# Kernel optimization log

Hardware: AMD Instinct MI355X
Metric: run time of the kernel (lower is better)

## Reference

```python
import jax, jax.numpy as jnp
import numpy as np

B, S, D_MODEL, H = 4, 2048, 1024, 16
D_K = D_MODEL // H


def setup_inputs() -> dict:
    key = jax.random.key(0)
    kx, kq, kk, kv, ko = jax.random.split(key, 5)
    scale = 1.0 / np.sqrt(D_MODEL)
    return {
        "x": jax.random.normal(kx, (B, S, D_MODEL), dtype=jnp.float32),
        "W_q": jax.random.normal(kq, (D_MODEL, D_MODEL), dtype=jnp.float32) * scale,
        "W_k": jax.random.normal(kk, (D_MODEL, D_MODEL), dtype=jnp.float32) * scale,
        "W_v": jax.random.normal(kv, (D_MODEL, D_MODEL), dtype=jnp.float32) * scale,
        "W_out": jax.random.normal(ko, (D_MODEL, D_MODEL), dtype=jnp.float32) * scale,
    }


def reference(x, W_q, W_k, W_v, W_out):
    # nn.Linear(bias=False): y = x @ W.T; weights stored as (out, in).
    Bx, Sx, D = x.shape
    q = (x @ W_q.T).reshape(Bx, Sx, H, D_K).transpose(0, 2, 1, 3)  # (B,H,S,d_k)
    k = (x @ W_k.T).reshape(Bx, Sx, H, D_K).transpose(0, 2, 1, 3)
    v = (x @ W_v.T).reshape(Bx, Sx, H, D_K).transpose(0, 2, 1, 3)
    scores = jnp.einsum("bhsd,bhtd->bhst", q, k) / jnp.sqrt(jnp.float32(D_K))
    attn = jax.nn.softmax(scores, axis=-1)
    out = jnp.einsum("bhst,bhtd->bhsd", attn, v)  # (B,H,S,d_k)
    out = out.transpose(0, 2, 1, 3).reshape(Bx, Sx, D)  # combine heads
    return out @ W_out.T
```

## Files before the change

### kernel.cpp

```cpp
#include <hip/hip_runtime.h>

#define BATCH 4
#define SEQ 2048
#define DM 1024
#define NH 16
#define DK 64

typedef unsigned short u16;
typedef unsigned int u32;
typedef __attribute__((ext_vector_type(8))) short bfrag;
typedef __attribute__((ext_vector_type(4))) short bfrag4;
typedef __attribute__((ext_vector_type(4))) float ffrag;

#if defined(__has_builtin)
#if __has_builtin(__builtin_amdgcn_mfma_f32_16x16x16bf16_1k)
#define HAVE_MFMA16 1
#endif
#endif
#ifndef HAVE_MFMA16
#define HAVE_MFMA16 0
#endif

__device__ inline u16 f2bf(float f) {
  union { float f; u32 u; } v; v.f = f;
  u32 u = v.u;
  return (u16)((u + 0x7FFFu + ((u >> 16) & 1u)) >> 16);
}
__device__ inline float bf2f(u16 u) {
  union { u32 u; float f; } v; v.u = ((u32)u) << 16;
  return v.f;
}
__device__ inline ffrag MFMA(bfrag a, bfrag b, ffrag c) {
  return __builtin_amdgcn_mfma_f32_16x16x32_bf16(a, b, c, 0, 0, 0);
}
#if HAVE_MFMA16
__device__ inline ffrag MFMA16(bfrag4 a, bfrag4 b, ffrag c) {
  return __builtin_amdgcn_mfma_f32_16x16x16bf16_1k(a, b, c, 0, 0, 0);
}
#endif

__device__ __forceinline__ void g2l16(const u16* g, u16* l) {
  __builtin_amdgcn_global_load_lds(
      (const __attribute__((address_space(1))) u16*)g,
      (__attribute__((address_space(3))) u16*)l, 16, 0, 0);
}

__global__ __launch_bounds__(256) void cvt_bf16(const float* __restrict__ in,
                                                u16* __restrict__ out, int n4) {
  int i = blockIdx.x * 256 + threadIdx.x;
  if (i >= n4) return;
  float4 v = ((const float4*)in)[i];
  union { u16 u[4]; uint2 d; } o;
  o.u[0] = f2bf(v.x); o.u[1] = f2bf(v.y); o.u[2] = f2bf(v.z); o.u[3] = f2bf(v.w);
  ((uint2*)out)[i] = o.d;
}

__global__ __launch_bounds__(256) void cvt_w4(
    const float* __restrict__ a, const float* __restrict__ b,
    const float* __restrict__ c, const float* __restrict__ d,
    u16* __restrict__ oa, u16* __restrict__ ob,
    u16* __restrict__ oc, u16* __restrict__ od) {
  int which = blockIdx.x >> 10;
  int i = (blockIdx.x & 1023) * 256 + threadIdx.x;
  const float* in = which == 0 ? a : which == 1 ? b : which == 2 ? c : d;
  u16* out = which == 0 ? oa : which == 1 ? ob : which == 2 ? oc : od;
  float4 v = ((const float4*)in)[i];
  union { u16 u[4]; uint2 dd; } o;
  o.u[0] = f2bf(v.x); o.u[1] = f2bf(v.y); o.u[2] = f2bf(v.z); o.u[3] = f2bf(v.w);
  ((uint2*)out)[i] = o.dd;
}

__global__ __launch_bounds__(256) void gemm_qkv(
    const u16* __restrict__ xb,
    const u16* __restrict__ Wq, const u16* __restrict__ Wk,
    u16* __restrict__ Qb, u16* __restrict__ Kb) {
  const u16* Bm; u16* O;
  if (blockIdx.z == 0) { Bm = Wq; O = Qb; }
  else { Bm = Wk; O = Kb; }

  const int K = DM;
  const int bm = blockIdx.y * 128, bn = blockIdx.x * 128;
  __shared__ __align__(16) u16 As[128 * 32];
  __shared__ __align__(16) u16 Bs[128 * 32];
  const int tid = threadIdx.x;
  const int lane = tid & 63;
  const int w = tid >> 6;
  const int wr = w >> 1, wc = w & 1;
  const int l15 = lane & 15, quad = lane >> 4;
  const int srow = tid >> 2, scol = (tid & 3) * 8;

  ffrag acc[4][4] = {};

  for (int k0 = 0; k0 < K; k0 += 32) {
    __syncthreads();
    g2l16(&xb[(size_t)(bm + srow) * K + k0 + scol], &As[tid * 8]);
    g2l16(&xb[(size_t)(bm + 64 + srow) * K + k0 + scol], &As[(tid + 256) * 8]);
    g2l16(&Bm[(size_t)(bn + srow) * K + k0 + scol], &Bs[tid * 8]);
    g2l16(&Bm[(size_t)(bn + 64 + srow) * K + k0 + scol], &Bs[(tid + 256) * 8]);
    __syncthreads();
    bfrag af[4], bf[4];
#pragma unroll
    for (int i = 0; i < 4; i++)
      af[i] = *(const bfrag*)(&As[(wr * 64 + i * 16 + l15) * 32 + quad * 8]);
#pragma unroll
    for (int j = 0; j < 4; j++)
      bf[j] = *(const bfrag*)(&Bs[(wc * 64 + j * 16 + l15) * 32 + quad * 8]);
#pragma unroll
    for (int i = 0; i < 4; i++)
#pragma unroll
      for (int j = 0; j < 4; j++)
        acc[i][j] = MFMA(af[i], bf[j], acc[i][j]);
  }

#pragma unroll
  for (int i = 0; i < 4; i++)
#pragma unroll
    for (int j = 0; j < 4; j++)
#pragma unroll
      for (int r = 0; r < 4; r++) {
        int m = bm + wr * 64 + i * 16 + quad * 4 + r;
        int n = bn + wc * 64 + j * 16 + l15;
        int b = m >> 11, s = m & 2047;
        int h = n >> 6, d = n & 63;
        O[(((size_t)(b * NH + h)) * SEQ + s) * DK + d] = f2bf(acc[i][j][r]);
      }
}

__global__ __launch_bounds__(256) void gemm_v(
    const u16* __restrict__ xb, const u16* __restrict__ Wv,
    u16* __restrict__ VbT) {
  const int K = DM;
  const int bm = blockIdx.y * 128, bn = blockIdx.x * 128;
  __shared__ __align__(16) u16 As[128 * 32];
  __shared__ __align__(16) u16 Bs[128 * 32];
  const int tid = threadIdx.x;
  const int lane = tid & 63;
  const int w = tid >> 6;
  const int wr = w >> 1, wc = w & 1;
  const int l15 = lane & 15, quad = lane >> 4;
  const int srow = tid >> 2, scol = (tid & 3) * 8;

  ffrag acc[4][4] = {};

  for (int k0 = 0; k0 < K; k0 += 32) {
    __syncthreads();
    g2l16(&xb[(size_t)(bm + srow) * K + k0 + scol], &As[tid * 8]);
    g2l16(&xb[(size_t)(bm + 64 + srow) * K + k0 + scol], &As[(tid + 256) * 8]);
    g2l16(&Wv[(size_t)(bn + srow) * K + k0 + scol], &Bs[tid * 8]);
    g2l16(&Wv[(size_t)(bn + 64 + srow) * K + k0 + scol], &Bs[(tid + 256) * 8]);
    __syncthreads();
    bfrag af[4], bf[4];
#pragma unroll
    for (int i = 0; i < 4; i++)
      af[i] = *(const bfrag*)(&Bs[(wr * 64 + i * 16 + l15) * 32 + quad * 8]);
#pragma unroll
    for (int j = 0; j < 4; j++)
      bf[j] = *(const bfrag*)(&As[(wc * 64 + j * 16 + l15) * 32 + quad * 8]);
#pragma unroll
    for (int i = 0; i < 4; i++)
#pragma unroll
      for (int j = 0; j < 4; j++)
        acc[i][j] = MFMA(af[i], bf[j], acc[i][j]);
  }

#pragma unroll
  for (int i = 0; i < 4; i++)
#pragma unroll
    for (int j = 0; j < 4; j++)
#pragma unroll
      for (int r = 0; r < 4; r++) {
        int n = bn + wr * 64 + i * 16 + quad * 4 + r;
        int m = bm + wc * 64 + j * 16 + l15;
        int b = m >> 11, s = m & 2047;
        int h = n >> 6, d = n & 63;
        VbT[(((size_t)(b * NH + h)) * DK + d) * SEQ + s] = f2bf(acc[i][j][r]);
      }
}

__global__ __launch_bounds__(256) void gemm_out(
    const u16* __restrict__ Ab, const u16* __restrict__ Wo, float* __restrict__ C) {
  const int K = DM, N = DM;
  const int bm = blockIdx.y * 128, bn = blockIdx.x * 128;
  __shared__ __align__(16) u16 As[128 * 32];
  __shared__ __align__(16) u16 Bs[128 * 32];
  const int tid = threadIdx.x;
  const int lane = tid & 63;
  const int w = tid >> 6;
  const int wr = w >> 1, wc = w & 1;
  const int l15 = lane & 15, quad = lane >> 4;
  const int srow = tid >> 2, scol = (tid & 3) * 8;

  ffrag acc[4][4] = {};

  for (int k0 = 0; k0 < K; k0 += 32) {
    __syncthreads();
    g2l16(&Ab[(size_t)(bm + srow) * K + k0 + scol], &As[tid * 8]);
    g2l16(&Ab[(size_t)(bm + 64 + srow) * K + k0 + scol], &As[(tid + 256) * 8]);
    g2l16(&Wo[(size_t)(bn + srow) * K + k0 + scol], &Bs[tid * 8]);
    g2l16(&Wo[(size_t)(bn + 64 + srow) * K + k0 + scol], &Bs[(tid + 256) * 8]);
    __syncthreads();
    bfrag af[4], bf[4];
#pragma unroll
    for (int i = 0; i < 4; i++)
      af[i] = *(const bfrag*)(&As[(wr * 64 + i * 16 + l15) * 32 + quad * 8]);
#pragma unroll
    for (int j = 0; j < 4; j++)
      bf[j] = *(const bfrag*)(&Bs[(wc * 64 + j * 16 + l15) * 32 + quad * 8]);
#pragma unroll
    for (int i = 0; i < 4; i++)
#pragma unroll
      for (int j = 0; j < 4; j++)
        acc[i][j] = MFMA(af[i], bf[j], acc[i][j]);
  }

#pragma unroll
  for (int i = 0; i < 4; i++)
#pragma unroll
    for (int j = 0; j < 4; j++)
#pragma unroll
      for (int r = 0; r < 4; r++) {
        int m = bm + wr * 64 + i * 16 + quad * 4 + r;
        int n = bn + wc * 64 + j * 16 + l15;
        C[(size_t)m * N + n] = acc[i][j][r];
      }
}

#define ATS 72
__global__ __launch_bounds__(256) void attn(
    const u16* __restrict__ Qb, const u16* __restrict__ Kb,
    const u16* __restrict__ VbT, u16* __restrict__ Ab) {
  const int bh = blockIdx.y;
  const int b = bh >> 4, h = bh & 15;
  const int qbase = blockIdx.x * 128;
  const int tid = threadIdx.x;
  const int w = tid >> 6, lane = tid & 63;
  const int l15 = lane & 15, quad = lane >> 4;

  __shared__ __align__(16) u16 Ks[64 * ATS];
  __shared__ __align__(16) u16 Vt[64 * ATS];
#if !HAVE_MFMA16
  __shared__ __align__(16) u16 Ps[4][32 * ATS];
#endif

  const size_t hbase = (size_t)bh * SEQ * DK;

  const float qscale = 0.125f * 1.4426950408889634f;
  bfrag q[2][2];
#pragma unroll
  for (int i = 0; i < 2; i++)
#pragma unroll
    for (int kk = 0; kk < 2; kk++) {
      bfrag t = *(const bfrag*)(&Qb[hbase +
          (size_t)(qbase + w * 32 + i * 16 + l15) * DK + kk * 32 + quad * 8]);
#pragma unroll
      for (int e = 0; e < 8; e++)
        q[i][kk][e] = (short)f2bf(bf2f((u16)t[e]) * qscale);
    }

  ffrag O[4][2] = {};
  float lsum[2] = {0.f, 0.f};

  for (int kv0 = 0; kv0 < SEQ; kv0 += 64) {
    __syncthreads();
#pragma unroll
    for (int i = 0; i < 2; i++) {
      int c = tid + i * 256;
      int row = c >> 3, col = (c & 7) * 8;
      *(int4*)(&Ks[row * ATS + col]) =
          *(const int4*)(&Kb[hbase + (size_t)(kv0 + row) * DK + col]);
      *(int4*)(&Vt[row * ATS + col]) =
          *(const int4*)(&VbT[hbase + (size_t)row * SEQ + kv0 + col]);
    }
    __syncthreads();

#if HAVE_MFMA16
    bfrag4 pb[4][2];
#endif
#pragma unroll
    for (int j = 0; j < 4; j++) {
      bfrag k0f = *(const bfrag*)(&Ks[(j * 16 + l15) * ATS + quad * 8]);
      bfrag k1f = *(const bfrag*)(&Ks[(j * 16 + l15) * ATS + 32 + quad * 8]);
#pragma unroll
      for (int i = 0; i < 2; i++) {
        ffrag z = {};
        z = MFMA(k0f, q[i][0], z);
        z = MFMA(k1f, q[i][1], z);
        u32 u[4]; float ts = 0.f;
#pragma unroll
        for (int r = 0; r < 4; r++) {
          float p = __builtin_amdgcn_exp2f(z[r]);
          u[r] = __float_as_uint(p);
          ts += __uint_as_float(u[r] & 0xffff0000u);
        }
        lsum[i] += ts;
        u32 lo = (u[1] & 0xffff0000u) | (u[0] >> 16);
        u32 hi = (u[3] & 0xffff0000u) | (u[2] >> 16);
#if HAVE_MFMA16
        union { u32 d[2]; bfrag4 v; } pk;
        pk.d[0] = lo; pk.d[1] = hi;
        pb[j][i] = pk.v;
#else
        union { u32 d[2]; uint2 v; } pk;
        pk.d[0] = lo; pk.d[1] = hi;
        *(uint2*)(&Ps[w][(i * 16 + l15) * ATS + j * 16 + quad * 4]) = pk.v;
#endif
      }
    }

#if HAVE_MFMA16
#pragma unroll
    for (int j = 0; j < 4; j++)
#pragma unroll
      for (int db = 0; db < 4; db++) {
        bfrag4 vf = *(const bfrag4*)(&Vt[(db * 16 + l15) * ATS + j * 16 + quad * 4]);
        O[db][0] = MFMA16(vf, pb[j][0], O[db][0]);
        O[db][1] = MFMA16(vf, pb[j][1], O[db][1]);
      }
#else
#pragma unroll
    for (int kk = 0; kk < 2; kk++) {
      bfrag pf0 = *(const bfrag*)(&Ps[w][l15 * ATS + kk * 32 + quad * 8]);
      bfrag pf1 = *(const bfrag*)(&Ps[w][(16 + l15) * ATS + kk * 32 + quad * 8]);
#pragma unroll
      for (int db = 0; db < 4; db++) {
        bfrag vf = *(const bfrag*)(&Vt[(db * 16 + l15) * ATS + kk * 32 + quad * 8]);
        O[db][0] = MFMA(vf, pf0, O[db][0]);
        O[db][1] = MFMA(vf, pf1, O[db][1]);
      }
    }
#endif
  }

  float rl[2];
#pragma unroll
  for (int i = 0; i < 2; i++) {
    float s = lsum[i];
    s += __shfl_xor(s, 16);
    s += __shfl_xor(s, 32);
    rl[i] = 1.0f / s;
  }

  const size_t obase = ((size_t)b * SEQ) * DM + (size_t)h * DK;
#pragma unroll
  for (int db = 0; db < 4; db++)
#pragma unroll
    for (int i = 0; i < 2; i++) {
      int s = qbase + w * 32 + i * 16 + l15;
      union { u16 u[4]; uint2 d; } o;
#pragma unroll
      for (int r = 0; r < 4; r++) o.u[r] = f2bf(O[db][i][r] * rl[i]);
      *(uint2*)(&Ab[obase + (size_t)s * DM + db * 16 + quad * 4]) = o.d;
    }
}

extern "C" void kernel_launch(void* const* d_in, const int* in_sizes, int n_in,
                              void* d_out, int out_size, void* d_ws, size_t ws_size,
                              hipStream_t stream) {
  const float* x  = (const float*)d_in[0];
  const float* Wq = (const float*)d_in[1];
  const float* Wk = (const float*)d_in[2];
  const float* Wv = (const float*)d_in[3];
  const float* Wo = (const float*)d_in[4];
  float* out = (float*)d_out;

  char* ws = (char*)d_ws;
  u16* xb  = (u16*)(ws + 0);
  u16* Wqb = (u16*)(ws + 16777216);
  u16* Wkb = (u16*)(ws + 18874368);
  u16* Wvb = (u16*)(ws + 20971520);
  u16* Wob = (u16*)(ws + 23068672);
  u16* Qb  = (u16*)(ws + 25165824);
  u16* Kb  = (u16*)(ws + 41943040);
  u16* VbT = (u16*)(ws + 58720256);
  u16* Ab  = (u16*)(ws + 75497472);
  const size_t NEED = 92274688;
  if (ws_size < NEED) return;

  cvt_bf16<<<8192, 256, 0, stream>>>(x, xb, (BATCH * SEQ * DM) / 4);
  cvt_w4<<<4096, 256, 0, stream>>>(Wq, Wk, Wv, Wo, Wqb, Wkb, Wvb, Wob);

  dim3 gqk(DM / 128, (BATCH * SEQ) / 128, 2);
  gemm_qkv<<<gqk, 256, 0, stream>>>(xb, Wqb, Wkb, Qb, Kb);
  dim3 gv(DM / 128, (BATCH * SEQ) / 128);
  gemm_v<<<gv, 256, 0, stream>>>(xb, Wvb, VbT);

  dim3 gat(SEQ / 128, BATCH * NH);
  attn<<<gat, 256, 0, stream>>>(Qb, Kb, VbT, Ab);

  dim3 gout(DM / 128, (BATCH * SEQ) / 128);
  gemm_out<<<gout, 256, 0, stream>>>(Ab, Wob, out);
}
```

Baseline: 309.7 us.

## Pre-swizzle V into MFMA fragment layout and double-buffer V via direct LDS loads

The V projection now writes V in a per-64-key-tile swizzled layout that matches the MFMA16 B-fragment order, so the attention kernel can copy each tile into LDS with contiguous global_load_lds and read fragments without padding. V tiles are double-buffered so the next tile's load overlaps the current compute, and K fragments are read straight from global memory instead of being staged in LDS. This removes the per-iteration register round-trip staging and one barrier, at the risk of uncoalesced, cache-reliant K loads. The non-MFMA16 fallback is removed and replaced with a stub that returns c unchanged.

Result: slower. 345.5 us (+11.6%).

```diff
diff --git a/kernel.cpp b/kernel.cpp
--- a/kernel.cpp
+++ b/kernel.cpp
@@ -12,31 +12,29 @@
 typedef __attribute__((ext_vector_type(4))) short bfrag4;
 typedef __attribute__((ext_vector_type(4))) float ffrag;
 
+__device__ inline u16 f2bf(float f) {
+  union { float f; u32 u; } v; v.f = f;
+  u32 u = v.u;
+  return (u16)((u + 0x7FFFu + ((u >> 16) & 1u)) >> 16);
+}
+__device__ inline float bf2f(u16 u) {
+  union { u32 u; float f; } v; v.u = ((u32)u) << 16;
+  return v.f;
+}
+__device__ inline ffrag MFMA(bfrag a, bfrag b, ffrag c) {
+  return __builtin_amdgcn_mfma_f32_16x16x32_bf16(a, b, c, 0, 0, 0);
+}
 #if defined(__has_builtin)
 #if __has_builtin(__builtin_amdgcn_mfma_f32_16x16x16bf16_1k)
 #define HAVE_MFMA16 1
 #endif
 #endif
-#ifndef HAVE_MFMA16
-#define HAVE_MFMA16 0
-#endif
-
-__device__ inline u16 f2bf(float f) {
-  union { float f; u32 u; } v; v.f = f;
-  u32 u = v.u;
-  return (u16)((u + 0x7FFFu + ((u >> 16) & 1u)) >> 16);
-}
-__device__ inline float bf2f(u16 u) {
-  union { u32 u; float f; } v; v.u = ((u32)u) << 16;
-  return v.f;
-}
-__device__ inline ffrag MFMA(bfrag a, bfrag b, ffrag c) {
-  return __builtin_amdgcn_mfma_f32_16x16x32_bf16(a, b, c, 0, 0, 0);
-}
 #if HAVE_MFMA16
 __device__ inline ffrag MFMA16(bfrag4 a, bfrag4 b, ffrag c) {
   return __builtin_amdgcn_mfma_f32_16x16x16bf16_1k(a, b, c, 0, 0, 0);
 }
+#else
+__device__ inline ffrag MFMA16(bfrag4 a, bfrag4 b, ffrag c) { return c; }
 #endif
 
 __device__ __forceinline__ void g2l16(const u16* g, u16* l) {
@@ -128,7 +126,7 @@
 
 __global__ __launch_bounds__(256) void gemm_v(
     const u16* __restrict__ xb, const u16* __restrict__ Wv,
-    u16* __restrict__ VbT) {
+    u16* __restrict__ Vsw) {
   const int K = DM;
   const int bm = blockIdx.y * 128, bn = blockIdx.x * 128;
   __shared__ __align__(16) u16 As[128 * 32];
@@ -173,7 +171,11 @@
         int m = bm + wc * 64 + j * 16 + l15;
         int b = m >> 11, s = m & 2047;
         int h = n >> 6, d = n & 63;
-        VbT[(((size_t)(b * NH + h)) * DK + d) * SEQ + s] = f2bf(acc[i][j][r]);
+        size_t hb = (size_t)(b * NH + h) * (SEQ * DK);
+        size_t off = hb + (size_t)(s >> 6) * 4096 +
+            ((((d >> 4) * 4 + ((s >> 4) & 3)) * 64 +
+              ((s >> 2) & 3) * 16 + (d & 15)) * 4 + (s & 3));
+        Vsw[off] = f2bf(acc[i][j][r]);
       }
 }
 
@@ -225,10 +227,9 @@
       }
 }
 
-#define ATS 72
 __global__ __launch_bounds__(256) void attn(
     const u16* __restrict__ Qb, const u16* __restrict__ Kb,
-    const u16* __restrict__ VbT, u16* __restrict__ Ab) {
+    const u16* __restrict__ Vsw, u16* __restrict__ Ab) {
   const int bh = blockIdx.y;
   const int b = bh >> 4, h = bh & 15;
   const int qbase = blockIdx.x * 128;
@@ -236,11 +237,7 @@
   const int w = tid >> 6, lane = tid & 63;
   const int l15 = lane & 15, quad = lane >> 4;
 
-  __shared__ __align__(16) u16 Ks[64 * ATS];
-  __shared__ __align__(16) u16 Vt[64 * ATS];
-#if !HAVE_MFMA16
-  __shared__ __align__(16) u16 Ps[4][32 * ATS];
-#endif
+  __shared__ __align__(16) u16 Vt[2][4096];
 
   const size_t hbase = (size_t)bh * SEQ * DK;
 
@@ -260,26 +257,28 @@
   ffrag O[4][2] = {};
   float lsum[2] = {0.f, 0.f};
 
-  for (int kv0 = 0; kv0 < SEQ; kv0 += 64) {
-    __syncthreads();
-#pragma unroll
-    for (int i = 0; i < 2; i++) {
-      int c = tid + i * 256;
-      int row = c >> 3, col = (c & 7) * 8;
-      *(int4*)(&Ks[row * ATS + col]) =
-          *(const int4*)(&Kb[hbase + (size_t)(kv0 + row) * DK + col]);
-      *(int4*)(&Vt[row * ATS + col]) =
-          *(const int4*)(&VbT[hbase + (size_t)row * SEQ + kv0 + col]);
+  {
+    const u16* src = &Vsw[hbase];
+    g2l16(&src[tid * 8], &Vt[0][tid * 8]);
+    g2l16(&src[2048 + tid * 8], &Vt[0][2048 + tid * 8]);
+  }
+
+  for (int t = 0; t < SEQ / 64; t++) {
+    const int kv0 = t * 64;
+    const int buf = t & 1;
+    __syncthreads();
+    if (t + 1 < SEQ / 64) {
+      const u16* src = &Vsw[hbase + (size_t)(t + 1) * 4096];
+      g2l16(&src[tid * 8], &Vt[buf ^ 1][tid * 8]);
+      g2l16(&src[2048 + tid * 8], &Vt[buf ^ 1][2048 + tid * 8]);
     }
-    __syncthreads();
-
-#if HAVE_MFMA16
+
     bfrag4 pb[4][2];
-#endif
 #pragma unroll
     for (int j = 0; j < 4; j++) {
-      bfrag k0f = *(const bfrag*)(&Ks[(j * 16 + l15) * ATS + quad * 8]);
-      bfrag k1f = *(const bfrag*)(&Ks[(j * 16 + l15) * ATS + 32 + quad * 8]);
+      const u16* krow = &Kb[hbase + (size_t)(kv0 + j * 16 + l15) * DK + quad * 8];
+      bfrag k0f = *(const bfrag*)(krow);
+      bfrag k1f = *(const bfrag*)(krow + 32);
 #pragma unroll
       for (int i = 0; i < 2; i++) {
         ffrag z = {};
@@ -293,42 +292,21 @@
           ts += __uint_as_float(u[r] & 0xffff0000u);
         }
         lsum[i] += ts;
-        u32 lo = (u[1] & 0xffff0000u) | (u[0] >> 16);
-        u32 hi = (u[3] & 0xffff0000u) | (u[2] >> 16);
-#if HAVE_MFMA16
         union { u32 d[2]; bfrag4 v; } pk;
-        pk.d[0] = lo; pk.d[1] = hi;
+        pk.d[0] = (u[1] & 0xffff0000u) | (u[0] >> 16);
+        pk.d[1] = (u[3] & 0xffff0000u) | (u[2] >> 16);
         pb[j][i] = pk.v;
-#else
-        union { u32 d[2]; uint2 v; } pk;
-        pk.d[0] = lo; pk.d[1] = hi;
-        *(uint2*)(&Ps[w][(i * 16 + l15) * ATS + j * 16 + quad * 4]) = pk.v;
-#endif
       }
     }
 
-#if HAVE_MFMA16
 #pragma unroll
     for (int j = 0; j < 4; j++)
 #pragma unroll
       for (int db = 0; db < 4; db++) {
-        bfrag4 vf = *(const bfrag4*)(&Vt[(db * 16 + l15) * ATS + j * 16 + quad * 4]);
+        bfrag4 vf = *(const bfrag4*)(&Vt[buf][((db * 4 + j) * 64 + lane) * 4]);
         O[db][0] = MFMA16(vf, pb[j][0], O[db][0]);
         O[db][1] = MFMA16(vf, pb[j][1], O[db][1]);
       }
-#else
-#pragma unroll
-    for (int kk = 0; kk < 2; kk++) {
-      bfrag pf0 = *(const bfrag*)(&Ps[w][l15 * ATS + kk * 32 + quad * 8]);
-      bfrag pf1 = *(const bfrag*)(&Ps[w][(16 + l15) * ATS + kk * 32 + quad * 8]);
-#pragma unroll
-      for (int db = 0; db < 4; db++) {
-        bfrag vf = *(const bfrag*)(&Vt[(db * 16 + l15) * ATS + kk * 32 + quad * 8]);
-        O[db][0] = MFMA(vf, pf0, O[db][0]);
-        O[db][1] = MFMA(vf, pf1, O[db][1]);
-      }
-    }
-#endif
   }
 
   float rl[2];
@@ -371,7 +349,7 @@
   u16* Wob = (u16*)(ws + 23068672);
   u16* Qb  = (u16*)(ws + 25165824);
   u16* Kb  = (u16*)(ws + 41943040);
-  u16* VbT = (u16*)(ws + 58720256);
+  u16* Vsw = (u16*)(ws + 58720256);
   u16* Ab  = (u16*)(ws + 75497472);
   const size_t NEED = 92274688;
   if (ws_size < NEED) return;
@@ -382,10 +360,10 @@
   dim3 gqk(DM / 128, (BATCH * SEQ) / 128, 2);
   gemm_qkv<<<gqk, 256, 0, stream>>>(xb, Wqb, Wkb, Qb, Kb);
   dim3 gv(DM / 128, (BATCH * SEQ) / 128);
-  gemm_v<<<gv, 256, 0, stream>>>(xb, Wvb, VbT);
+  gemm_v<<<gv, 256, 0, stream>>>(xb, Wvb, Vsw);
 
   dim3 gat(SEQ / 128, BATCH * NH);
-  attn<<<gat, 256, 0, stream>>>(Qb, Kb, VbT, Ab);
+  attn<<<gat, 256, 0, stream>>>(Qb, Kb, Vsw, Ab);
 
   dim3 gout(DM / 128, (BATCH * SEQ) / 128);
   gemm_out<<<gout, 256, 0, stream>>>(Ab, Wob, out);
```
